# Kernel tuning notes

Measured on AMD Instinct MI355X. Metric: run time of the kernel, lower is better.

The kernel has to match this reference:

```python
import jax, jax.numpy as jnp
import numpy as np

B, T, C, H = 2, 2048, 1024, 16
HD = C // H  # 64
EPS = 1e-5


def _ln(x, g, b):
    mu = jnp.mean(x, axis=-1, keepdims=True)
    var = jnp.var(x, axis=-1, keepdims=True)
    return (x - mu) * jax.lax.rsqrt(var + EPS) * g + b


def setup_inputs() -> dict:
    key = jax.random.key(0)
    ks = jax.random.split(key, 8)
    s = lambda n: 1.0 / np.sqrt(n)
    return {
        "x": jax.random.normal(ks[0], (B, T, C), dtype=jnp.float32),
        "ln1_g": jnp.ones((C,), jnp.float32), "ln1_b": jnp.zeros((C,), jnp.float32),
        "ln2_g": jnp.ones((C,), jnp.float32), "ln2_b": jnp.zeros((C,), jnp.float32),
        "w_in": jax.random.normal(ks[1], (C, 3 * C), jnp.float32) * s(C),
        "b_in": jnp.zeros((3 * C,), jnp.float32),
        "w_out": jax.random.normal(ks[2], (C, C), jnp.float32) * s(C),
        "b_out": jnp.zeros((C,), jnp.float32),
        "w_fc": jax.random.normal(ks[3], (C, 4 * C), jnp.float32) * s(C),
        "b_fc": jnp.zeros((4 * C,), jnp.float32),
        "w_proj": jax.random.normal(ks[4], (4 * C, C), jnp.float32) * s(4 * C),
        "b_proj": jnp.zeros((C,), jnp.float32),
    }


def reference(x, ln1_g, ln1_b, ln2_g, ln2_b, w_in, b_in, w_out, b_out,
              w_fc, b_fc, w_proj, b_proj):
    # --- residual 1: x + attn(ln1(x)) ---
    h = _ln(x, ln1_g, ln1_b)
    qkv = h @ w_in + b_in                          # (B,T,3C)
    # reshape to (B,T,H,3*HD) then chunk per head (matches torch code exactly)
    qkv = qkv.reshape(B, T, H, 3 * HD).transpose(0, 2, 1, 3)  # (B,H,T,3*HD)
    q, k, v = jnp.split(qkv, 3, axis=-1)           # each (B,H,T,HD)
    att = jnp.einsum('bhqd,bhkd->bhqk', q, k) / np.sqrt(HD)
    causal = jnp.tril(jnp.ones((T, T), bool))
    att = jnp.where(causal, att, -jnp.inf)
    att = jax.nn.softmax(att, axis=-1)
    o = jnp.einsum('bhqk,bhkd->bhqd', att, v)      # (B,H,T,HD)
    o = o.transpose(0, 2, 1, 3).reshape(B, T, C)
    x1 = x + (o @ w_out + b_out)
    # --- ln2 applied to residual stream, then residual 2 on top of ln2 output ---
    y = _ln(x1, ln2_g, ln2_b)
    mlp = jax.nn.gelu(y @ w_fc + b_fc, approximate=False) @ w_proj + b_proj
    return y + mlp
```

## Files before the change

### kernel.cpp

```cpp
#include <hip/hip_runtime.h>
#include <hip/hip_bf16.h>
#include <math.h>

typedef __bf16 bf16;
typedef __bf16 bf16x8 __attribute__((ext_vector_type(8)));
typedef __bf16 bf16x4 __attribute__((ext_vector_type(4)));
typedef float floatx4 __attribute__((ext_vector_type(4)));

#define B_ 2
#define T_ 2048
#define C_ 1024
#define H_ 16
#define HD_ 64

__device__ __forceinline__ void gload_lds16(const bf16* g, bf16* l) {
    __builtin_amdgcn_global_load_lds(
        (const __attribute__((address_space(1))) unsigned int*)(g),
        (__attribute__((address_space(3))) unsigned int*)(l), 16, 0, 0);
}

__global__ __launch_bounds__(256) void transpose_all(
        const float* __restrict__ w_in, const float* __restrict__ w_out,
        const float* __restrict__ w_fc, const float* __restrict__ w_proj,
        bf16* __restrict__ o_in, bf16* __restrict__ o_out,
        bf16* __restrict__ o_fc, bf16* __restrict__ o_proj) {
    __shared__ float shf[32 * 33];
    int t = blockIdx.x;
    int tid = threadIdx.x;
    const float* src; bf16* dst; int K, N, idx;
    if (t < 3072)      { src = w_in;   dst = o_in;   K = 1024; N = 3072; idx = t; }
    else if (t < 7168) { src = w_fc;   dst = o_fc;   K = 1024; N = 4096; idx = t - 3072; }
    else if (t < 8192) { src = w_out;  dst = o_out;  K = 1024; N = 1024; idx = t - 7168; }
    else               { src = w_proj; dst = o_proj; K = 4096; N = 1024; idx = t - 8192; }
    int ntx = N >> 5;
    int nt = (idx % ntx) * 32, kt = (idx / ntx) * 32;
    int tx = tid & 31, ty = tid >> 5;
    #pragma unroll
    for (int i = 0; i < 32; i += 8)
        shf[(ty + i) * 33 + tx] = src[(size_t)(kt + ty + i) * N + nt + tx];
    __syncthreads();
    #pragma unroll
    for (int i = 0; i < 32; i += 8)
        dst[(size_t)(nt + ty + i) * K + kt + tx] = (bf16)shf[tx * 33 + ty + i];
}

__global__ __launch_bounds__(256) void ln_kernel(const float* __restrict__ x,
                                                 const float* __restrict__ g,
                                                 const float* __restrict__ b,
                                                 bf16* __restrict__ out_b,
                                                 float* __restrict__ out_f) {
    int row = blockIdx.x;
    int tid = threadIdx.x;
    const float* xr = x + (size_t)row * C_;
    float4 v = ((const float4*)xr)[tid];
    float s  = v.x + v.y + v.z + v.w;
    float ss = v.x * v.x + v.y * v.y + v.z * v.z + v.w * v.w;
    #pragma unroll
    for (int off = 32; off; off >>= 1) {
        s  += __shfl_down(s, off);
        ss += __shfl_down(ss, off);
    }
    __shared__ float red[8];
    int wid = tid >> 6;
    if ((tid & 63) == 0) { red[wid] = s; red[wid + 4] = ss; }
    __syncthreads();
    s  = red[0] + red[1] + red[2] + red[3];
    ss = red[4] + red[5] + red[6] + red[7];
    float mean = s * (1.0f / C_);
    float var  = ss * (1.0f / C_) - mean * mean;
    float rstd = rsqrtf(var + 1e-5f);
    float4 gv = ((const float4*)g)[tid];
    float4 bv = ((const float4*)b)[tid];
    float o0 = (v.x - mean) * rstd * gv.x + bv.x;
    float o1 = (v.y - mean) * rstd * gv.y + bv.y;
    float o2 = (v.z - mean) * rstd * gv.z + bv.z;
    float o3 = (v.w - mean) * rstd * gv.w + bv.w;
    bf16x4 ob = { (bf16)o0, (bf16)o1, (bf16)o2, (bf16)o3 };
    ((bf16x4*)out_b)[(size_t)row * 256 + tid] = ob;
    if (out_f) {
        float4 of; of.x = o0; of.y = o1; of.z = o2; of.w = o3;
        ((float4*)out_f)[(size_t)row * 256 + tid] = of;
    }
}

__device__ __forceinline__ float gelu_fast(float x) {
    float z2 = 1.5957691216f * (x + 0.044715f * x * x * x);
    float e = __expf(z2);
    float t = 1.0f - 2.0f * __builtin_amdgcn_rcpf(e + 1.0f);
    return 0.5f * x * (1.0f + t);
}

#define BAR() do { __builtin_amdgcn_sched_barrier(0); __builtin_amdgcn_s_barrier(); __builtin_amdgcn_sched_barrier(0); } while (0)
#define VMC6() asm volatile("s_waitcnt vmcnt(6)" ::: "memory")
#define VMC0() asm volatile("s_waitcnt vmcnt(0)" ::: "memory")

#define LOAD_A(AS, QM) \
  { _Pragma("unroll") for (int i_ = 0; i_ < 4; i_++) { \
      const int r_ = wm128 + ((QM) * 4 + i_) * 16 + lm; \
      _Pragma("unroll") for (int kc_ = 0; kc_ < 2; kc_++) \
        aR[i_][kc_] = *(const bf16x8*)((AS) + r_ * 64 + ((((kc_ << 2) | quad) ^ (lm & 7)) << 3)); } }

#define LOAD_B(BS, QN) \
  { _Pragma("unroll") for (int j_ = 0; j_ < 2; j_++) { \
      const int r_ = wn64 + ((QN) * 2 + j_) * 16 + lm; \
      _Pragma("unroll") for (int kc_ = 0; kc_ < 2; kc_++) \
        bR[QN][j_][kc_] = *(const bf16x8*)((BS) + r_ * 64 + ((((kc_ << 2) | quad) ^ (lm & 7)) << 3)); } }

#define MFMA_Q(QM, QN) \
  { __builtin_amdgcn_s_setprio(1); \
    _Pragma("unroll") for (int i_ = 0; i_ < 4; i_++) \
    _Pragma("unroll") for (int j_ = 0; j_ < 2; j_++) \
    _Pragma("unroll") for (int kc_ = 0; kc_ < 2; kc_++) \
      acc[(QM) * 4 + i_][(QN) * 2 + j_] = __builtin_amdgcn_mfma_f32_16x16x32_bf16( \
          aR[i_][kc_], bR[QN][j_][kc_], acc[(QM) * 4 + i_][(QN) * 2 + j_], 0, 0, 0); \
    __builtin_amdgcn_s_setprio(0); }

#define STG(gb, lb, r0v, k0v) \
    gload_lds16((gb) + (size_t)((r0v) + sr8) * K + (k0v) + scb, (lb) + ((r0v) + wid * 8) * 64)

template<int MODE>
__global__ __launch_bounds__(512, 2) void gemm256(const bf16* __restrict__ A,
                                                  const bf16* __restrict__ Bt,
                                                  const float* __restrict__ bias,
                                                  void* __restrict__ out,
                                                  int M, int N, int K) {
    (void)M;
    __shared__ __align__(16) bf16 smem[4 * 256 * 64];
    bf16* As0 = smem;
    bf16* Bs0 = smem + 1 * 256 * 64;
    bf16* As1 = smem + 2 * 256 * 64;
    bf16* Bs1 = smem + 3 * 256 * 64;

    int ntn = N >> 8;
    int lin = blockIdx.x;
    int id  = (lin & 7) * (gridDim.x >> 3) + (lin >> 3);
    int mt = id / ntn, nt = id - mt * ntn;
    int m0 = mt << 8, n0 = nt << 8;

    int tid = threadIdx.x;
    int wid = __builtin_amdgcn_readfirstlane(tid >> 6);
    int lane = tid & 63;
    int lm = lane & 15, quad = lane >> 4;
    int wm128 = (wid & 1) * 128;
    int wn64  = (wid >> 1) * 64;

    const bf16* Ablk = A  + (size_t)m0 * K;
    const bf16* Bblk = Bt + (size_t)n0 * K;

    int sr8 = wid * 8 + (lane >> 3);
    int scb = ((lane & 7) ^ (lane >> 3)) << 3;

    floatx4 acc[8][4];
    #pragma unroll
    for (int f = 0; f < 8; f++)
        #pragma unroll
        for (int g = 0; g < 4; g++) { floatx4 z = {0.f, 0.f, 0.f, 0.f}; acc[f][g] = z; }
    bf16x8 aR[4][2], bR[2][2][2];

    int nI = K >> 7;

    STG(Ablk, As0, 0, 0);   STG(Ablk, As0, 64, 0);
    STG(Ablk, As0, 128, 0); STG(Ablk, As0, 192, 0);
    STG(Bblk, Bs0, 0, 0);   STG(Bblk, Bs0, 64, 0);
    STG(Bblk, Bs0, 128, 0); STG(Bblk, Bs0, 192, 0);
    STG(Ablk, As1, 0, 64);  STG(Ablk, As1, 128, 64);
    STG(Bblk, Bs1, 0, 64);  STG(Bblk, Bs1, 64, 64);
    STG(Ablk, As1, 64, 64); STG(Ablk, As1, 192, 64);
    VMC6();
    BAR();

    for (int it = 0; it < nI; it++) {
        int kE = (2 * it + 2) << 6;
        int kO = (2 * it + 3) << 6;
        int kT = (2 * it + 1) << 6;
        bool nl = (it + 1 < nI);
        LOAD_A(As0, 0); LOAD_B(Bs0, 0);
        STG(Bblk, Bs1, 128, kT); STG(Bblk, Bs1, 192, kT);
        BAR(); MFMA_Q(0, 0); BAR();
        LOAD_B(Bs0, 1);
        if (nl) { STG(Ablk, As0, 0, kE); STG(Ablk, As0, 128, kE); }
        BAR(); MFMA_Q(0, 1); BAR();
        LOAD_A(As0, 1);
        if (nl) { STG(Bblk, Bs0, 0, kE); STG(Bblk, Bs0, 64, kE); }
        BAR(); MFMA_Q(1, 0); BAR();
        if (nl) { STG(Ablk, As0, 64, kE); STG(Ablk, As0, 192, kE); }
        BAR(); MFMA_Q(1, 1);
        if (nl) { VMC6(); } else { VMC0(); }
        BAR();
        LOAD_A(As1, 0); LOAD_B(Bs1, 0);
        if (nl) { STG(Bblk, Bs0, 128, kE); STG(Bblk, Bs0, 192, kE); }
        BAR(); MFMA_Q(0, 0); BAR();
        LOAD_B(Bs1, 1);
        if (nl) { STG(Ablk, As1, 0, kO); STG(Ablk, As1, 128, kO); }
        BAR(); MFMA_Q(0, 1); BAR();
        LOAD_A(As1, 1);
        if (nl) { STG(Bblk, Bs1, 0, kO); STG(Bblk, Bs1, 64, kO); }
        BAR(); MFMA_Q(1, 0); BAR();
        if (nl) { STG(Ablk, As1, 64, kO); STG(Ablk, As1, 192, kO); }
        BAR(); MFMA_Q(1, 1);
        if (nl) { VMC6(); }
        BAR();
    }

    if (MODE == 0) {
        bf16* ob = (bf16*)out;
        #pragma unroll
        for (int f = 0; f < 8; f++) {
            int row0 = m0 + wm128 + f * 16 + quad * 4;
            #pragma unroll
            for (int g = 0; g < 4; g++) {
                int n = n0 + wn64 + g * 16 + lm;
                float bsn = bias[n];
                #pragma unroll
                for (int r = 0; r < 4; r++)
                    ob[(size_t)(row0 + r) * N + n] = (bf16)(acc[f][g][r] + bsn);
            }
        }
    } else {
        bf16* ob = (bf16*)out;
        bf16* patch = smem + wid * (64 * 68);
        #pragma unroll
        for (int h = 0; h < 2; h++) {
            #pragma unroll
            for (int ff = 0; ff < 4; ff++)
                #pragma unroll
                for (int g = 0; g < 4; g++) {
                    int n = n0 + wn64 + g * 16 + lm;
                    float bsn = bias[n];
                    #pragma unroll
                    for (int r = 0; r < 4; r++)
                        patch[(ff * 16 + quad * 4 + r) * 68 + g * 16 + lm] =
                            (bf16)gelu_fast(acc[h * 4 + ff][g][r] + bsn);
                }
            #pragma unroll
            for (int ff = 0; ff < 4; ff++)
                #pragma unroll
                for (int kc = 0; kc < 2; kc++) {
                    bf16x8 v = *(const bf16x8*)&patch[(ff * 16 + lm) * 68 + kc * 32 + quad * 8];
                    size_t row = (size_t)(m0 + wm128 + h * 64 + ff * 16 + lm);
                    *(bf16x8*)(ob + row * N + n0 + wn64 + kc * 32 + quad * 8) = v;
                }
        }
    }
}

#define VMCP(n) asm volatile("s_waitcnt vmcnt(" #n ")" ::: "memory")

#define STGP(kt) { bf16* bs_ = smem + ((kt) & 3) * 16384; \
    gload_lds16(Ab + (size_t)sr8 * K + (kt) * 64 + scb,        bs_ + (wid * 8) * 64); \
    gload_lds16(Ab + (size_t)(64 + sr8) * K + (kt) * 64 + scb, bs_ + (64 + wid * 8) * 64); \
    gload_lds16(Bb + (size_t)sr8 * K + (kt) * 64 + scb,        bs_ + 8192 + (wid * 8) * 64); \
    gload_lds16(Bb + (size_t)(64 + sr8) * K + (kt) * 64 + scb, bs_ + 8192 + (64 + wid * 8) * 64); }

__global__ __launch_bounds__(512, 2) void gemm_npipe(const bf16* __restrict__ A,
                                                     const bf16* __restrict__ Bt,
                                                     const float* __restrict__ bias,
                                                     const float* __restrict__ add,
                                                     float* __restrict__ out,
                                                     int N, int K) {
    __shared__ __align__(16) bf16 smem[4 * 16384];
    int lin = blockIdx.x;
    int xcd = lin & 7, loc = lin >> 3;
    int m0 = (xcd * 4 + (loc & 3)) * 128;
    int n0 = (loc >> 2) * 128;
    int tid = threadIdx.x;
    int wid = __builtin_amdgcn_readfirstlane(tid >> 6);
    int lane = tid & 63;
    int lm = lane & 15, quad = lane >> 4;
    int wm32 = (wid & 3) * 32, wn64 = (wid >> 2) * 64;
    int sr8 = wid * 8 + (lane >> 3);
    int scb = ((lane & 7) ^ (lane >> 3)) << 3;
    const bf16* Ab = A  + (size_t)m0 * K;
    const bf16* Bb = Bt + (size_t)n0 * K;
    int NT = K >> 6;

    floatx4 acc[2][4];
    #pragma unroll
    for (int i = 0; i < 2; i++)
        #pragma unroll
        for (int j = 0; j < 4; j++) { floatx4 z = {0.f, 0.f, 0.f, 0.f}; acc[i][j] = z; }
    bf16x8 aR[2][2], bR[4][2];

    STGP(0); STGP(1); STGP(2);
    VMCP(8);
    BAR();

    for (int t = 0; t < NT; t++) {
        if (t + 3 < NT) STGP(t + 3);
        bf16* bs = smem + (t & 3) * 16384;
        #pragma unroll
        for (int i = 0; i < 2; i++)
            #pragma unroll
            for (int kc = 0; kc < 2; kc++)
                aR[i][kc] = *(const bf16x8*)(bs + (wm32 + i * 16 + lm) * 64 +
                                             ((((kc << 2) | quad) ^ (lm & 7)) << 3));
        #pragma unroll
        for (int j = 0; j < 4; j++)
            #pragma unroll
            for (int kc = 0; kc < 2; kc++)
                bR[j][kc] = *(const bf16x8*)(bs + 8192 + (wn64 + j * 16 + lm) * 64 +
                                             ((((kc << 2) | quad) ^ (lm & 7)) << 3));
        __builtin_amdgcn_s_setprio(1);
        #pragma unroll
        for (int kc = 0; kc < 2; kc++)
            #pragma unroll
            for (int i = 0; i < 2; i++)
                #pragma unroll
                for (int j = 0; j < 4; j++)
                    acc[i][j] = __builtin_amdgcn_mfma_f32_16x16x32_bf16(
                        aR[i][kc], bR[j][kc], acc[i][j], 0, 0, 0);
        __builtin_amdgcn_s_setprio(0);
        if (t + 3 < NT)      { VMCP(8); }
        else if (t == NT - 3){ VMCP(4); }
        else if (t == NT - 2){ VMCP(0); }
        BAR();
    }

    #pragma unroll
    for (int i = 0; i < 2; i++)
        #pragma unroll
        for (int j = 0; j < 4; j++) {
            int mbase = m0 + wm32 + i * 16 + quad * 4;
            int n     = n0 + wn64 + j * 16 + lm;
            float bsn = bias[n];
            #pragma unroll
            for (int r = 0; r < 4; r++) {
                size_t idx = (size_t)(mbase + r) * N + n;
                out[idx] = acc[i][j][r] + bsn + add[idx];
            }
        }
}

#define QT_ 128
#define KT_ 64

__global__ __launch_bounds__(512) void attn_mfma_kernel(const bf16* __restrict__ qkv,
                                                        bf16* __restrict__ of) {
    int bh = blockIdx.x;
    int b = bh >> 4, h = bh & 15;
    int q0 = (gridDim.y - 1 - blockIdx.y) * QT_;
    int tid = threadIdx.x, wid = tid >> 6, lane = tid & 63;
    int lm = lane & 15, quad = lane >> 4;
    int sw = lm & 7;
    int r0 = q0 + wid * 16;

    const bf16* base = qkv + (size_t)b * T_ * (3 * C_) + h * (3 * HD_);

    __shared__ __align__(16) bf16 Ks[KT_][72];
    __shared__ __align__(16) bf16 Vt[HD_][72];
    __shared__ __align__(16) bf16 PsT[8][16][64];

    bf16x8 qf[2];
    #pragma unroll
    for (int kc = 0; kc < 2; kc++) {
        bf16x8 t = *(const bf16x8*)(base + (size_t)(r0 + lm) * (3 * C_) + kc * 32 + quad * 8);
        #pragma unroll
        for (int e = 0; e < 8; e++) t[e] = (bf16)((float)t[e] * 0.125f);
        qf[kc] = t;
    }

    floatx4 acc_o[4];
    #pragma unroll
    for (int dn = 0; dn < 4; dn++) { floatx4 z = {0.f, 0.f, 0.f, 0.f}; acc_o[dn] = z; }
    float mst = -1e30f, lst = 0.0f;

    int srow = tid >> 3;
    int scol = (tid & 7) * 8;

    int kmax = q0 + QT_;
    for (int k0 = 0; k0 < kmax; k0 += KT_) {
        bf16x8 kv = *(const bf16x8*)(base + (size_t)(k0 + srow) * (3 * C_) + HD_ + scol);
        bf16x8 vv = *(const bf16x8*)(base + (size_t)(k0 + srow) * (3 * C_) + 2 * HD_ + scol);
        __syncthreads();
        *(bf16x8*)(&Ks[srow][scol]) = kv;
        {
            int c = scol >> 3;
            int pk = ((srow >> 3) ^ c) * 8 + (srow & 7);
            #pragma unroll
            for (int j = 0; j < 8; j++) Vt[scol + j][pk] = vv[j];
        }
        __syncthreads();

        if (k0 <= r0 + 15) {
            floatx4 st[4];
            #pragma unroll
            for (int bn = 0; bn < 4; bn++) { floatx4 z = {0.f, 0.f, 0.f, 0.f}; st[bn] = z; }
            #pragma unroll
            for (int kc = 0; kc < 2; kc++) {
                bf16x8 kf[4];
                #pragma unroll
                for (int bn = 0; bn < 4; bn++)
                    kf[bn] = *(const bf16x8*)(&Ks[bn * 16 + lm][kc * 32 + quad * 8]);
                __builtin_amdgcn_s_setprio(1);
                #pragma unroll
                for (int bn = 0; bn < 4; bn++)
                    st[bn] = __builtin_amdgcn_mfma_f32_16x16x32_bf16(kf[bn], qf[kc], st[bn], 0, 0, 0);
                __builtin_amdgcn_s_setprio(0);
            }

            float vv_[4][4];
            float rm = -1e30f;
            if (k0 + KT_ - 1 > r0) {
                int gq = r0 + lm;
                #pragma unroll
                for (int bn = 0; bn < 4; bn++)
                    #pragma unroll
                    for (int r = 0; r < 4; r++) {
                        int key = k0 + bn * 16 + quad * 4 + r;
                        float sv = (key <= gq) ? st[bn][r] : -1e30f;
                        vv_[bn][r] = sv;
                        rm = fmaxf(rm, sv);
                    }
            } else {
                #pragma unroll
                for (int bn = 0; bn < 4; bn++)
                    #pragma unroll
                    for (int r = 0; r < 4; r++) {
                        vv_[bn][r] = st[bn][r];
                        rm = fmaxf(rm, st[bn][r]);
                    }
            }
            rm = fmaxf(rm, __shfl_xor(rm, 16));
            rm = fmaxf(rm, __shfl_xor(rm, 32));
            float mnew = fmaxf(mst, rm);
            float alpha = __expf(mst - mnew);
            mst = mnew;
            float ps = 0.f;
            #pragma unroll
            for (int bn = 0; bn < 4; bn++) {
                float p0 = __expf(vv_[bn][0] - mnew);
                float p1 = __expf(vv_[bn][1] - mnew);
                float p2 = __expf(vv_[bn][2] - mnew);
                float p3 = __expf(vv_[bn][3] - mnew);
                ps += (p0 + p1) + (p2 + p3);
                bf16x4 pk = { (bf16)p0, (bf16)p1, (bf16)p2, (bf16)p3 };
                int kb = bn * 2 + (quad >> 1);
                int col = ((kb ^ sw) << 3) + (quad & 1) * 4;
                *(bf16x4*)(&PsT[wid][lm][col]) = pk;
            }
            ps += __shfl_xor(ps, 16);
            ps += __shfl_xor(ps, 32);
            lst = lst * alpha + ps;

            #pragma unroll
            for (int r = 0; r < 4; r++) {
                float ar = __shfl(alpha, quad * 4 + r);
                #pragma unroll
                for (int dn = 0; dn < 4; dn++) acc_o[dn][r] *= ar;
            }

            __asm__ volatile("s_waitcnt lgkmcnt(0)" ::: "memory");

            #pragma unroll
            for (int kc = 0; kc < 2; kc++) {
                bf16x8 pa = *(const bf16x8*)(&PsT[wid][lm][((kc * 4 + quad) ^ sw) << 3]);
                bf16x8 vfr[4];
                #pragma unroll
                for (int dn = 0; dn < 4; dn++) {
                    int d = dn * 16 + lm;
                    int swd = (d >> 3) & 7;
                    vfr[dn] = *(const bf16x8*)(&Vt[d][(((kc * 4 + quad) ^ swd) << 3)]);
                }
                __builtin_amdgcn_s_setprio(1);
                #pragma unroll
                for (int dn = 0; dn < 4; dn++)
                    acc_o[dn] = __builtin_amdgcn_mfma_f32_16x16x32_bf16(pa, vfr[dn], acc_o[dn], 0, 0, 0);
                __builtin_amdgcn_s_setprio(0);
            }
        }
    }

    float il = 1.0f / lst;
    #pragma unroll
    for (int r = 0; r < 4; r++) {
        float ir = __shfl(il, quad * 4 + r);
        #pragma unroll
        for (int dn = 0; dn < 4; dn++)
            PsT[wid][quad * 4 + r][dn * 16 + lm] = (bf16)(acc_o[dn][r] * ir);
    }
    __asm__ volatile("s_waitcnt lgkmcnt(0)" ::: "memory");
    size_t rowg = (size_t)b * T_ + r0 + lm;
    #pragma unroll
    for (int kcl = 0; kcl < 2; kcl++) {
        bf16x8 v = *(const bf16x8*)&PsT[wid][lm][kcl * 32 + quad * 8];
        *(bf16x8*)(of + rowg * C_ + h * HD_ + kcl * 32 + quad * 8) = v;
    }
}

extern "C" void kernel_launch(void* const* d_in, const int* in_sizes, int n_in,
                              void* d_out, int out_size, void* d_ws, size_t ws_size,
                              hipStream_t stream) {
    (void)in_sizes; (void)n_in; (void)out_size; (void)ws_size;
    const float* x      = (const float*)d_in[0];
    const float* ln1_g  = (const float*)d_in[1];
    const float* ln1_b  = (const float*)d_in[2];
    const float* ln2_g  = (const float*)d_in[3];
    const float* ln2_b  = (const float*)d_in[4];
    const float* w_in   = (const float*)d_in[5];
    const float* b_in   = (const float*)d_in[6];
    const float* w_out  = (const float*)d_in[7];
    const float* b_out  = (const float*)d_in[8];
    const float* w_fc   = (const float*)d_in[9];
    const float* b_fc   = (const float*)d_in[10];
    const float* w_proj = (const float*)d_in[11];
    const float* b_proj = (const float*)d_in[12];

    char* ws = (char*)d_ws;
    const size_t MB = 1024 * 1024;
    bf16*  w_inT   = (bf16*)(ws + 0);
    bf16*  w_outT  = (bf16*)(ws + 6 * MB);
    bf16*  w_fcT   = (bf16*)(ws + 8 * MB);
    bf16*  w_projT = (bf16*)(ws + 16 * MB);
    bf16*  qkv     = (bf16*)(ws + 24 * MB);
    bf16*  fc_b    = (bf16*)(ws + 24 * MB);
    bf16*  o_b     = (bf16*)(ws + 56 * MB);
    bf16*  y_b     = (bf16*)(ws + 56 * MB);
    bf16*  h_b     = (bf16*)(ws + 64 * MB);
    float* x1      = (float*)(ws + 64 * MB);
    float* y_f     = (float*)(ws + 80 * MB);

    const int M = B_ * T_;

    transpose_all<<<12288, 256, 0, stream>>>(w_in, w_out, w_fc, w_proj,
                                             w_inT, w_outT, w_fcT, w_projT);

    ln_kernel<<<M, 256, 0, stream>>>(x, ln1_g, ln1_b, h_b, nullptr);
    gemm256<0><<<(M >> 8) * ((3 * C_) >> 8), 512, 0, stream>>>(h_b, w_inT, b_in,
                                                               qkv, M, 3 * C_, C_);
    attn_mfma_kernel<<<dim3(B_ * H_, T_ / QT_), 512, 0, stream>>>(qkv, o_b);
    gemm_npipe<<<256, 512, 0, stream>>>(o_b, w_outT, b_out, x, x1, C_, C_);
    ln_kernel<<<M, 256, 0, stream>>>(x1, ln2_g, ln2_b, y_b, y_f);
    gemm256<1><<<(M >> 8) * ((4 * C_) >> 8), 512, 0, stream>>>(y_b, w_fcT, b_fc,
                                                               fc_b, M, 4 * C_, C_);
    gemm_npipe<<<256, 512, 0, stream>>>(fc_b, w_projT, b_proj, y_f,
                                        (float*)d_out, C_, 4 * C_);
}
```

Baseline: 319.6 us.

## Double-buffer K/V tiles in attention with async LDS loads and shuffle transpose

The attention kernel now keeps two K and V tile buffers in shared memory. The next K tile is prefetched with global_load_lds straight into a swizzled buffer, and the next V tile is loaded into registers while the current tile is computed, which removes one of the two barriers per iteration. The V transpose now exchanges pairs of rows with a lane shuffle and writes 32-bit words instead of 8 scalar bf16 stores. The grid-y order is also remapped to interleave long and short causal blocks, and the wave id is made uniform with readfirstlane. The cost is more shared memory (fewer blocks per CU) and more complex indexing.

```diff
diff --git a/kernel.cpp b/kernel.cpp
--- a/kernel.cpp
+++ b/kernel.cpp
@@ -6,6 +6,7 @@
 typedef __bf16 bf16x8 __attribute__((ext_vector_type(8)));
 typedef __bf16 bf16x4 __attribute__((ext_vector_type(4)));
 typedef float floatx4 __attribute__((ext_vector_type(4)));
+typedef int intx4 __attribute__((ext_vector_type(4)));
 
 #define B_ 2
 #define T_ 2048
@@ -334,20 +335,45 @@
 #define QT_ 128
 #define KT_ 64
 
+__device__ __forceinline__ void vt_stage(bf16* VtB, bf16x8 vv, int vdb,
+                                         int vcolb, int oddf) {
+    intx4 vi = *(intx4*)&vv;
+    intx4 pi;
+    #pragma unroll
+    for (int m = 0; m < 4; m++) pi[m] = __shfl_xor(vi[m], 8);
+    #pragma unroll
+    for (int j = 0; j < 4; j++) {
+        int w0 = j >> 1, sh = (j & 1) * 16;
+        unsigned int oe = ((unsigned int)vi[w0] >> sh) & 0xffffu;
+        unsigned int pe = ((unsigned int)pi[w0] >> sh) & 0xffffu;
+        unsigned int oo = ((unsigned int)vi[2 + w0] >> sh) & 0xffffu;
+        unsigned int po = ((unsigned int)pi[2 + w0] >> sh) & 0xffffu;
+        unsigned int de = oe | (pe << 16);
+        unsigned int dn = po | (oo << 16);
+        unsigned int dw = oddf ? dn : de;
+        *(unsigned int*)(VtB + (size_t)(vdb + j) * 72 + vcolb) = dw;
+    }
+}
+
 __global__ __launch_bounds__(512) void attn_mfma_kernel(const bf16* __restrict__ qkv,
                                                         bf16* __restrict__ of) {
     int bh = blockIdx.x;
     int b = bh >> 4, h = bh & 15;
-    int q0 = (gridDim.y - 1 - blockIdx.y) * QT_;
-    int tid = threadIdx.x, wid = tid >> 6, lane = tid & 63;
+    int ny = gridDim.y;
+    int gy = blockIdx.y;
+    int yy = (gy < (ny >> 1)) ? gy : (ny + (ny >> 1) - 1 - gy);
+    int q0 = (ny - 1 - yy) * QT_;
+    int tid = threadIdx.x;
+    int wid = __builtin_amdgcn_readfirstlane(tid >> 6);
+    int lane = tid & 63;
     int lm = lane & 15, quad = lane >> 4;
     int sw = lm & 7;
     int r0 = q0 + wid * 16;
 
     const bf16* base = qkv + (size_t)b * T_ * (3 * C_) + h * (3 * HD_);
 
-    __shared__ __align__(16) bf16 Ks[KT_][72];
-    __shared__ __align__(16) bf16 Vt[HD_][72];
+    __shared__ __align__(16) bf16 Ks[2][KT_][64];
+    __shared__ __align__(16) bf16 Vt[2][HD_][72];
     __shared__ __align__(16) bf16 PsT[8][16][64];
 
     bf16x8 qf[2];
@@ -365,22 +391,33 @@
     float mst = -1e30f, lst = 0.0f;
 
     int srow = tid >> 3;
+    int scb  = ((lane & 7) ^ (lane >> 3)) << 3;
     int scol = (tid & 7) * 8;
-
-    int kmax = q0 + QT_;
-    for (int k0 = 0; k0 < kmax; k0 += KT_) {
-        bf16x8 kv = *(const bf16x8*)(base + (size_t)(k0 + srow) * (3 * C_) + HD_ + scol);
-        bf16x8 vv = *(const bf16x8*)(base + (size_t)(k0 + srow) * (3 * C_) + 2 * HD_ + scol);
+    int oddf = srow & 1;
+    int vcolb = (((srow >> 3) ^ (tid & 7)) << 3) + (srow & 6);
+    int vdb   = scol + (oddf ? 4 : 0);
+
+    int ntiles = q0 / KT_ + 2;
+
+    {
+        gload_lds16(base + (size_t)srow * (3 * C_) + HD_ + scb, &Ks[0][wid * 8][0]);
+        bf16x8 vv = *(const bf16x8*)(base + (size_t)srow * (3 * C_) + 2 * HD_ + scol);
+        vt_stage(&Vt[0][0][0], vv, vdb, vcolb, oddf);
         __syncthreads();
-        *(bf16x8*)(&Ks[srow][scol]) = kv;
-        {
-            int c = scol >> 3;
-            int pk = ((srow >> 3) ^ c) * 8 + (srow & 7);
-            #pragma unroll
-            for (int j = 0; j < 8; j++) Vt[scol + j][pk] = vv[j];
+    }
+
+    for (int t = 0; t < ntiles; t++) {
+        int cur = t & 1;
+        bool pre = (t + 1 < ntiles);
+        bf16x8 vv;
+        if (pre) {
+            size_t nrow = (size_t)((t + 1) * KT_ + srow) * (3 * C_);
+            gload_lds16(base + nrow + HD_ + scb, &Ks[cur ^ 1][wid * 8][0]);
+            vv = *(const bf16x8*)(base + nrow + 2 * HD_ + scol);
         }
-        __syncthreads();
-
+        __builtin_amdgcn_sched_barrier(0);
+
+        int k0 = t * KT_;
         if (k0 <= r0 + 15) {
             floatx4 st[4];
             #pragma unroll
@@ -390,7 +427,8 @@
                 bf16x8 kf[4];
                 #pragma unroll
                 for (int bn = 0; bn < 4; bn++)
-                    kf[bn] = *(const bf16x8*)(&Ks[bn * 16 + lm][kc * 32 + quad * 8]);
+                    kf[bn] = *(const bf16x8*)(&Ks[cur][bn * 16 + lm]
+                                              [((((kc << 2) | quad) ^ sw) << 3)]);
                 __builtin_amdgcn_s_setprio(1);
                 #pragma unroll
                 for (int bn = 0; bn < 4; bn++)
@@ -459,7 +497,7 @@
                 for (int dn = 0; dn < 4; dn++) {
                     int d = dn * 16 + lm;
                     int swd = (d >> 3) & 7;
-                    vfr[dn] = *(const bf16x8*)(&Vt[d][(((kc * 4 + quad) ^ swd) << 3)]);
+                    vfr[dn] = *(const bf16x8*)(&Vt[cur][d][(((kc * 4 + quad) ^ swd) << 3)]);
                 }
                 __builtin_amdgcn_s_setprio(1);
                 #pragma unroll
@@ -468,6 +506,9 @@
                 __builtin_amdgcn_s_setprio(0);
             }
         }
+
+        if (pre) vt_stage(&Vt[cur ^ 1][0][0], vv, vdb, vcolb, oddf);
+        __syncthreads();
     }
 
     float il = 1.0f / lst;
```

Result: no change. 314.7 us (-1.5%).
